# Kernel tuning notes

Measured on AMD Instinct MI355X. Metric: run time of the kernel, lower is better.

## Reference

```python
import jax, jax.numpy as jnp
import numpy as np

DIM = 1024
DEPTH = 4
HEADS = 16
MLP = 4096
B, N = 4, 1024
SCALE = DIM ** (-0.5)  # NOTE: module scales by dim^-0.5, not head_dim^-0.5
EPS = 1e-5


def setup_inputs() -> dict:
    key = jax.random.key(0)
    ks = jax.random.split(key, 13)
    s = 0.02
    return {
        "x": jax.random.normal(ks[0], (B, N, DIM), dtype=jnp.float32),
        "ln1_g": jnp.ones((DEPTH, DIM), jnp.float32),
        "ln1_b": jnp.zeros((DEPTH, DIM), jnp.float32),
        "w_qkv": jax.random.normal(ks[1], (DEPTH, DIM, 3 * DIM), jnp.float32) * s,
        "w_out": jax.random.normal(ks[2], (DEPTH, DIM, DIM), jnp.float32) * s,
        "b_out": jnp.zeros((DEPTH, DIM), jnp.float32),
        "ln2_g": jnp.ones((DEPTH, DIM), jnp.float32),
        "ln2_b": jnp.zeros((DEPTH, DIM), jnp.float32),
        "w1": jax.random.normal(ks[3], (DEPTH, DIM, MLP), jnp.float32) * s,
        "b1": jnp.zeros((DEPTH, MLP), jnp.float32),
        "w2": jax.random.normal(ks[4], (DEPTH, MLP, DIM), jnp.float32) * s,
        "b2": jnp.zeros((DEPTH, DIM), jnp.float32),
    }


def _layernorm(x, g, b):
    m = jnp.mean(x, axis=-1, keepdims=True)
    v = jnp.mean(jnp.square(x - m), axis=-1, keepdims=True)
    return (x - m) * jax.lax.rsqrt(v + EPS) * g + b


def _gelu(x):
    # x * 0.5 * (1 + erf(x / sqrt(2)))  (exact GeLu from the module)
    return x * 0.5 * (1.0 + jax.lax.erf(x / jnp.sqrt(2.0).astype(x.dtype)))


def _block(x, p):
    ln1_g, ln1_b, w_qkv, w_out, b_out, ln2_g, ln2_b, w1, b1, w2, b2 = p
    # --- attention (pre-norm, residual) ---
    h = _layernorm(x, ln1_g, ln1_b)
    qkv = h @ w_qkv  # [b, n, 3*dim]
    q, k, v = jnp.split(qkv, 3, axis=-1)
    def heads(t):  # [b, n, dim] -> [b, h, n, d]
        b_, n_, _ = t.shape
        return t.reshape(b_, n_, HEADS, DIM // HEADS).transpose(0, 2, 1, 3)
    q, k, v = heads(q), heads(k), heads(v)
    dots = jnp.einsum('bhid,bhjd->bhij', q, k) * SCALE
    attn = jax.nn.softmax(dots, axis=-1)
    o = jnp.einsum('bhij,bhjd->bhid', attn, v)
    o = o.transpose(0, 2, 1, 3).reshape(x.shape)  # [b, n, dim]
    x = x + (o @ w_out + b_out)
    # --- feed-forward (pre-norm, residual) ---
    h = _layernorm(x, ln2_g, ln2_b)
    x = x + (_gelu(h @ w1 + b1) @ w2 + b2)
    return x


def reference(x, ln1_g, ln1_b, w_qkv, w_out, b_out, ln2_g, ln2_b, w1, b1, w2, b2):
    for l in range(DEPTH):
        p = (ln1_g[l], ln1_b[l], w_qkv[l], w_out[l], b_out[l],
             ln2_g[l], ln2_b[l], w1[l], b1[l], w2[l], b2[l])
        x = _block(x, p)
    return x
```

## Files before the change

kernel.cpp:

```cpp
#include <hip/hip_runtime.h>

typedef __bf16 bf16;
typedef __bf16 bf16x4 __attribute__((ext_vector_type(4)));
typedef __bf16 bf16x8 __attribute__((ext_vector_type(8)));
typedef float  f32x4  __attribute__((ext_vector_type(4)));

#define DIMV   1024
#define MLPV   4096
#define MROWS  4096
#define NHEAD  16
#define SCALEV 0.03125f
#define QKV_LD 3072
#define MB (1024ull * 1024ull)

__device__ __forceinline__ void gload16(const bf16* g, bf16* l) {
    __builtin_amdgcn_global_load_lds((const __attribute__((address_space(1))) unsigned int*)g,
                                     (__attribute__((address_space(3))) unsigned int*)l,
                                     16, 0, 0);
}

__global__ __launch_bounds__(256) void k_ln(const float* __restrict__ x,
                                            const float* __restrict__ g,
                                            const float* __restrict__ b,
                                            bf16* __restrict__ h) {
    int row = blockIdx.x;
    int tid = threadIdx.x;
    const f32x4 v = ((const f32x4*)(x + (size_t)row * DIMV))[tid];
    float s  = v[0]+v[1]+v[2]+v[3];
    float sq = v[0]*v[0]+v[1]*v[1]+v[2]*v[2]+v[3]*v[3];
    for (int m = 1; m < 64; m <<= 1) { s += __shfl_xor(s, m, 64); sq += __shfl_xor(sq, m, 64); }
    __shared__ float ss[4], ssq[4];
    int w = tid >> 6, lane = tid & 63;
    if (lane == 0) { ss[w] = s; ssq[w] = sq; }
    __syncthreads();
    s  = ss[0]+ss[1]+ss[2]+ss[3];
    sq = ssq[0]+ssq[1]+ssq[2]+ssq[3];
    float mean = s * (1.f/DIMV);
    float var  = sq * (1.f/DIMV) - mean*mean;
    float rs   = rsqrtf(var + 1e-5f);
    int c0 = tid * 4;
    const f32x4 gv = ((const f32x4*)(g))[tid];
    const f32x4 bv = ((const f32x4*)(b))[tid];
    bf16x4 o;
    for (int i = 0; i < 4; i++)
        o[i] = (bf16)((v[i]-mean)*rs*gv[i] + bv[i]);
    *(bf16x4*)(h + (size_t)row * DIMV + c0) = o;
}

__global__ __launch_bounds__(256) void k_transpose_cvt(const float* __restrict__ in,
                                                       bf16* __restrict__ out, int R, int C) {
    __shared__ float tile[32][33];
    int tx = threadIdx.x & 31, ty = threadIdx.x >> 5;
    int r0 = blockIdx.y * 32, c0 = blockIdx.x * 32;
    for (int i = 0; i < 4; i++)
        tile[ty + 8*i][tx] = in[(size_t)(r0 + ty + 8*i) * C + c0 + tx];
    __syncthreads();
    for (int i = 0; i < 4; i++)
        out[(size_t)(c0 + ty + 8*i) * R + r0 + tx] = (bf16)tile[tx][ty + 8*i];
}

template<int EPI, int TN>
__global__ __launch_bounds__(256) void k_gemm(const bf16* __restrict__ A,
                                              const bf16* __restrict__ Bt,
                                              const float* __restrict__ bias,
                                              bf16* __restrict__ Cb,
                                              float* __restrict__ Cacc,
                                              int N, int K) {
    constexpr int NWN = TN / 64;
    constexpr int MT  = (TN == 128) ? 4 : 2;
    __shared__ alignas(16) bf16 As[2][128 * 64];
    __shared__ alignas(16) bf16 Bs[2][TN * 64];
    const int tid  = threadIdx.x;
    const int lane = tid & 63, w = tid >> 6;
    const int quad = lane >> 4, l16 = lane & 15;
    const int wm = w / NWN, wn = w % NWN;

    const int gx   = (int)gridDim.x;
    const int nwg  = gx * (int)gridDim.y;
    const int orig = (int)blockIdx.y * gx + (int)blockIdx.x;
    const int qq = nwg >> 3, rr = nwg & 7;
    const int xcd = orig & 7, loc = orig >> 3;
    const int wg  = (xcd < rr ? xcd * (qq + 1) : rr * (qq + 1) + (xcd - rr) * qq) + loc;
    const int bn = wg % gx, bm = wg / gx;

    const bf16* Ag = A  + (size_t)bm * 128 * K;
    const bf16* Bg = Bt + (size_t)bn * TN * K;

    const int srow = lane >> 3;
    const int scol = lane & 7;
    const int sswz = (scol ^ srow) << 3;

    f32x4 acc[MT][4];
    f32x4 zero = {0.f,0.f,0.f,0.f};
    for (int mt = 0; mt < MT; mt++) for (int nt = 0; nt < 4; nt++) acc[mt][nt] = zero;

    auto stage = [&](int p, int k0) {
        #pragma unroll
        for (int i = 0; i < 4; i++) {
            int row = w * 32 + i * 8;
            gload16(&Ag[(size_t)(row + srow) * K + k0 + sswz], &As[p][row * 64]);
        }
        #pragma unroll
        for (int i = 0; i < TN / 32; i++) {
            int row = w * (TN / 4) + i * 8;
            gload16(&Bg[(size_t)(row + srow) * K + k0 + sswz], &Bs[p][row * 64]);
        }
    };

    const int NT = K >> 6;
    stage(0, 0);
    __syncthreads();

    for (int t = 0; t < NT; t++) {
        const int p = t & 1;
        if (t + 1 < NT) stage(p ^ 1, (t + 1) << 6);

        bf16x8 af[MT][2], bfr[4][2];
        #pragma unroll
        for (int mt = 0; mt < MT; mt++)
            #pragma unroll
            for (int ks = 0; ks < 2; ks++) {
                int row = wm * (MT * 16) + mt * 16 + l16;
                int kb  = ks * 4 + quad;
                af[mt][ks] = *(const bf16x8*)&As[p][row * 64 + ((kb ^ (row & 7)) << 3)];
            }
        #pragma unroll
        for (int nt = 0; nt < 4; nt++)
            #pragma unroll
            for (int ks = 0; ks < 2; ks++) {
                int row = wn * 64 + nt * 16 + l16;
                int kb  = ks * 4 + quad;
                bfr[nt][ks] = *(const bf16x8*)&Bs[p][row * 64 + ((kb ^ (row & 7)) << 3)];
            }
        #pragma unroll
        for (int ks = 0; ks < 2; ks++)
            #pragma unroll
            for (int mt = 0; mt < MT; mt++)
                #pragma unroll
                for (int nt = 0; nt < 4; nt++)
                    acc[mt][nt] = __builtin_amdgcn_mfma_f32_16x16x32_bf16(af[mt][ks], bfr[nt][ks], acc[mt][nt], 0, 0, 0);

        __syncthreads();
    }

    for (int mt = 0; mt < MT; mt++) for (int nt = 0; nt < 4; nt++) {
        int col = bn * TN + wn * 64 + nt * 16 + l16;
        float bval = (EPI >= 1) ? bias[col] : 0.f;
        for (int r = 0; r < 4; r++) {
            int row = bm * 128 + wm * (MT * 16) + mt * 16 + quad * 4 + r;
            float v = acc[mt][nt][r];
            if (EPI == 0) {
                Cb[(size_t)row * N + col] = (bf16)v;
            } else if (EPI == 1) {
                float t = v + bval;
                float ge = 0.5f * t * (1.f + erff(t * 0.70710678118f));
                Cb[(size_t)row * N + col] = (bf16)ge;
            } else {
                Cacc[(size_t)row * N + col] += v + bval;
            }
        }
    }
}

__global__ __launch_bounds__(256) void k_attn(const bf16* __restrict__ qkv, bf16* __restrict__ o) {
    const int qt = blockIdx.x;
    const int h  = blockIdx.y;
    const int bb = blockIdx.z;
    const int tid  = threadIdx.x;
    const int lane = tid & 63, w = tid >> 6;
    const int quad = lane >> 4, l16 = lane & 15;

    __shared__ alignas(16) bf16 Qs[128 * 72];
    __shared__ alignas(16) bf16 Ks[64 * 72];
    __shared__ alignas(16) bf16 Vt[64 * 72];
    __shared__ alignas(16) bf16 Ps[128 * 72];

    const bf16* qbase = qkv + (size_t)(bb*1024 + qt*128) * QKV_LD + h*64;

    for (int c = tid; c < 1024; c += 256) {
        int r = c >> 3, cb = (c & 7) * 8;
        *(bf16x8*)&Qs[r * 72 + cb] = *(const bf16x8*)&qbase[(size_t)r * QKV_LD + cb];
    }

    f32x4 o_acc[2][4];
    f32x4 zero = {0.f,0.f,0.f,0.f};
    for (int mt = 0; mt < 2; mt++) for (int nt = 0; nt < 4; nt++) o_acc[mt][nt] = zero;
    float l_st[2][4];
    for (int mt = 0; mt < 2; mt++) for (int r = 0; r < 4; r++) l_st[mt][r] = 0.f;

    const int vj = tid >> 2;
    const int vd0 = (tid & 3) * 16;

    for (int kt = 0; kt < 16; kt++) {
        const bf16* kbase = qkv + (size_t)(bb*1024 + kt*64) * QKV_LD + 1024 + h*64;
        const bf16* vbase = qkv + (size_t)(bb*1024 + kt*64) * QKV_LD + 2048 + h*64;
        for (int c = tid; c < 512; c += 256) {
            int r = c >> 3, cb = (c & 7) * 8;
            *(bf16x8*)&Ks[r * 72 + cb] = *(const bf16x8*)&kbase[(size_t)r * QKV_LD + cb];
        }
        {
            bf16x8 v0 = *(const bf16x8*)&vbase[(size_t)vj * QKV_LD + vd0];
            bf16x8 v1 = *(const bf16x8*)&vbase[(size_t)vj * QKV_LD + vd0 + 8];
            #pragma unroll
            for (int i = 0; i < 8; i++) {
                Vt[(vd0 + i) * 72 + vj]     = v0[i];
                Vt[(vd0 + 8 + i) * 72 + vj] = v1[i];
            }
        }
        __syncthreads();

        f32x4 sv[2][4];
        for (int mt = 0; mt < 2; mt++) for (int nt = 0; nt < 4; nt++) {
            f32x4 a = zero;
            for (int ks = 0; ks < 2; ks++) {
                bf16x8 qf = *(const bf16x8*)&Qs[(w*32 + mt*16 + l16) * 72 + ks*32 + quad*8];
                bf16x8 kf = *(const bf16x8*)&Ks[(nt*16 + l16) * 72 + ks*32 + quad*8];
                a = __builtin_amdgcn_mfma_f32_16x16x32_bf16(qf, kf, a, 0, 0, 0);
            }
            for (int r = 0; r < 4; r++) sv[mt][nt][r] = a[r] * SCALEV;
        }

        for (int mt = 0; mt < 2; mt++) for (int r = 0; r < 4; r++) {
            float rs = 0.f;
            for (int nt = 0; nt < 4; nt++) {
                float p = __expf(sv[mt][nt][r]);
                sv[mt][nt][r] = p;
                rs += p;
            }
            for (int msk = 1; msk < 16; msk <<= 1) rs += __shfl_xor(rs, msk, 64);
            l_st[mt][r] += rs;
        }

        for (int mt = 0; mt < 2; mt++) for (int nt = 0; nt < 4; nt++)
            for (int r = 0; r < 4; r++)
                Ps[(w*32 + mt*16 + quad*4 + r) * 72 + nt*16 + l16] = (bf16)sv[mt][nt][r];
        __syncthreads();

        for (int mt = 0; mt < 2; mt++) for (int nt = 0; nt < 4; nt++) {
            f32x4 a = o_acc[mt][nt];
            for (int ks = 0; ks < 2; ks++) {
                bf16x8 pf = *(const bf16x8*)&Ps[(w*32 + mt*16 + l16) * 72 + ks*32 + quad*8];
                bf16x8 vf = *(const bf16x8*)&Vt[(nt*16 + l16) * 72 + ks*32 + quad*8];
                a = __builtin_amdgcn_mfma_f32_16x16x32_bf16(pf, vf, a, 0, 0, 0);
            }
            o_acc[mt][nt] = a;
        }
        __syncthreads();
    }

    for (int mt = 0; mt < 2; mt++) for (int nt = 0; nt < 4; nt++)
        for (int r = 0; r < 4; r++) {
            float val = o_acc[mt][nt][r] / l_st[mt][r];
            int row = qt*128 + w*32 + mt*16 + quad*4 + r;
            o[(size_t)(bb*1024 + row) * DIMV + h*64 + nt*16 + l16] = (bf16)val;
        }
}

extern "C" void kernel_launch(void* const* d_in, const int* in_sizes, int n_in,
                              void* d_out, int out_size, void* d_ws, size_t ws_size,
                              hipStream_t stream) {
    (void)in_sizes; (void)n_in; (void)out_size;
    const float* x_in  = (const float*)d_in[0];
    const float* ln1_g = (const float*)d_in[1];
    const float* ln1_b = (const float*)d_in[2];
    const float* w_qkv = (const float*)d_in[3];
    const float* w_out = (const float*)d_in[4];
    const float* b_out = (const float*)d_in[5];
    const float* ln2_g = (const float*)d_in[6];
    const float* ln2_b = (const float*)d_in[7];
    const float* w1    = (const float*)d_in[8];
    const float* b1    = (const float*)d_in[9];
    const float* w2    = (const float*)d_in[10];
    const float* b2    = (const float*)d_in[11];

    char* ws = (char*)d_ws;
    float* xf32    = (float*)ws;
    bf16*  h       = (bf16*)(ws + 16*MB);
    bf16*  wT1     = (bf16*)(ws + 24*MB);
    bf16*  wT2     = (bf16*)(ws + 32*MB);
    bf16*  attn_o  = (bf16*)(ws + 40*MB);
    bf16*  big     = (bf16*)(ws + 48*MB);
    size_t bigsz   = (ws_size > 48*MB) ? (ws_size - 48*MB) : 0;

    int G = 4;
    while (G > 1 && (size_t)G * 6*MB > bigsz) G >>= 1;
    int RC = 4096;
    while (RC > 128 && (size_t)RC * 8192ull > bigsz) RC >>= 1;

    hipMemcpyAsync(xf32, x_in, (size_t)MROWS * DIMV * sizeof(float),
                   hipMemcpyDeviceToDevice, stream);

    for (int l = 0; l < 4; l++) {
        k_ln<<<MROWS, 256, 0, stream>>>(xf32, ln1_g + (size_t)l*DIMV, ln1_b + (size_t)l*DIMV, h);
        k_transpose_cvt<<<dim3(3072/32, 1024/32), 256, 0, stream>>>(w_qkv + (size_t)l*DIMV*3072, wT1, 1024, 3072);
        for (int g = 0; g < 4; g += G) {
            k_gemm<0,128><<<dim3(3072/128, (G*1024)/128), 256, 0, stream>>>(
                h + (size_t)g*1024*DIMV, wT1, (const float*)nullptr, big, (float*)nullptr, 3072, 1024);
            k_attn<<<dim3(8, NHEAD, G), 256, 0, stream>>>(big, attn_o + (size_t)g*1024*DIMV);
        }
        k_transpose_cvt<<<dim3(1024/32, 1024/32), 256, 0, stream>>>(w_out + (size_t)l*DIMV*DIMV, wT1, 1024, 1024);
        k_gemm<2,64><<<dim3(1024/64, 4096/128), 256, 0, stream>>>(
            attn_o, wT1, b_out + (size_t)l*DIMV, (bf16*)nullptr, xf32, 1024, 1024);

        k_ln<<<MROWS, 256, 0, stream>>>(xf32, ln2_g + (size_t)l*DIMV, ln2_b + (size_t)l*DIMV, h);
        k_transpose_cvt<<<dim3(4096/32, 1024/32), 256, 0, stream>>>(w1 + (size_t)l*DIMV*MLPV, wT1, 1024, 4096);
        k_transpose_cvt<<<dim3(1024/32, 4096/32), 256, 0, stream>>>(w2 + (size_t)l*MLPV*DIMV, wT2, 4096, 1024);
        for (int r0 = 0; r0 < 4096; r0 += RC) {
            k_gemm<1,128><<<dim3(4096/128, RC/128), 256, 0, stream>>>(
                h + (size_t)r0*DIMV, wT1, b1 + (size_t)l*MLPV, big, (float*)nullptr, 4096, 1024);
            k_gemm<2,64><<<dim3(1024/64, RC/128), 256, 0, stream>>>(
                big, wT2, b2 + (size_t)l*DIMV, (bf16*)nullptr, xf32 + (size_t)r0*DIMV, 1024, 4096);
        }
    }

    hipMemcpyAsync(d_out, xf32, (size_t)MROWS * DIMV * sizeof(float),
                   hipMemcpyDeviceToDevice, stream);
}
```

Before: 1.265 ms.

## Pre-transpose V and double-buffer K/V with async LDS loads in attention

Adds a separate kernel that transposes V into a head-major buffer so the attention kernel no longer does a scalar scatter transpose into shared memory. The attention kernel now stages Q, K and V through direct global-to-LDS loads into XOR-swizzled tiles and double-buffers K/V so the next tile's loads overlap the current tile's MFMA work. It also drops one barrier and raises wave priority around the MFMA sections. In exchange it costs an extra kernel launch and a round trip of V through global memory, needs more workspace, and the barrier removal depends on the lgkmcnt wait alone ordering the Ps writes before they are read.

```diff
diff --git a/kernel.cpp b/kernel.cpp
--- a/kernel.cpp
+++ b/kernel.cpp
@@ -57,6 +57,19 @@
     __syncthreads();
     for (int i = 0; i < 4; i++)
         out[(size_t)(c0 + ty + 8*i) * R + r0 + tx] = (bf16)tile[tx][ty + 8*i];
+}
+
+__global__ __launch_bounds__(256) void k_vt(const bf16* __restrict__ big, bf16* __restrict__ vT) {
+    __shared__ bf16 tile[32][33];
+    int tx = threadIdx.x & 31, ty = threadIdx.x >> 5;
+    int hd0 = blockIdx.x * 32, s0 = blockIdx.y * 32, bb = blockIdx.z;
+    const bf16* src = big + (size_t)bb * 1024 * QKV_LD + 2048;
+    for (int i = 0; i < 4; i++)
+        tile[ty + 8*i][tx] = src[(size_t)(s0 + ty + 8*i) * QKV_LD + hd0 + tx];
+    __syncthreads();
+    bf16* dst = vT + (size_t)bb * 1024 * 1024;
+    for (int i = 0; i < 4; i++)
+        dst[(size_t)(hd0 + ty + 8*i) * 1024 + s0 + tx] = tile[tx][ty + 8*i];
 }
 
 template<int EPI, int TN>
@@ -162,25 +175,40 @@
     }
 }
 
-__global__ __launch_bounds__(256) void k_attn(const bf16* __restrict__ qkv, bf16* __restrict__ o) {
+__global__ __launch_bounds__(256) void k_attn(const bf16* __restrict__ qkv,
+                                              const bf16* __restrict__ vT,
+                                              bf16* __restrict__ o) {
     const int qt = blockIdx.x;
     const int h  = blockIdx.y;
     const int bb = blockIdx.z;
     const int tid  = threadIdx.x;
     const int lane = tid & 63, w = tid >> 6;
     const int quad = lane >> 4, l16 = lane & 15;
-
-    __shared__ alignas(16) bf16 Qs[128 * 72];
-    __shared__ alignas(16) bf16 Ks[64 * 72];
-    __shared__ alignas(16) bf16 Vt[64 * 72];
+    const int srow = lane >> 3, scol = lane & 7;
+    const int sswz = (scol ^ srow) << 3;
+
+    __shared__ alignas(16) bf16 Qs[128 * 64];
+    __shared__ alignas(16) bf16 Ks[2][64 * 64];
+    __shared__ alignas(16) bf16 Vs[2][64 * 64];
     __shared__ alignas(16) bf16 Ps[128 * 72];
 
-    const bf16* qbase = qkv + (size_t)(bb*1024 + qt*128) * QKV_LD + h*64;
-
-    for (int c = tid; c < 1024; c += 256) {
-        int r = c >> 3, cb = (c & 7) * 8;
-        *(bf16x8*)&Qs[r * 72 + cb] = *(const bf16x8*)&qbase[(size_t)r * QKV_LD + cb];
-    }
+    const bf16* qbase  = qkv + (size_t)(bb*1024 + qt*128) * QKV_LD + h*64;
+    const bf16* kbase0 = qkv + (size_t)(bb*1024) * QKV_LD + 1024 + h*64;
+    const bf16* vbase0 = vT  + ((size_t)bb*1024 + h*64) * 1024;
+
+    #pragma unroll
+    for (int i = 0; i < 4; i++) {
+        int row = w * 32 + i * 8;
+        gload16(&qbase[(size_t)(row + srow) * QKV_LD + sswz], &Qs[row * 64]);
+    }
+    auto stageKV = [&](int p, int kt) {
+        #pragma unroll
+        for (int i = 0; i < 2; i++) {
+            int row = w * 16 + i * 8;
+            gload16(&kbase0[(size_t)(kt*64 + row + srow) * QKV_LD + sswz], &Ks[p][row * 64]);
+            gload16(&vbase0[(size_t)(row + srow) * 1024 + kt*64 + sswz],   &Vs[p][row * 64]);
+        }
+    };
 
     f32x4 o_acc[2][4];
     f32x4 zero = {0.f,0.f,0.f,0.f};
@@ -188,44 +216,34 @@
     float l_st[2][4];
     for (int mt = 0; mt < 2; mt++) for (int r = 0; r < 4; r++) l_st[mt][r] = 0.f;
 
-    const int vj = tid >> 2;
-    const int vd0 = (tid & 3) * 16;
+    stageKV(0, 0);
+    __syncthreads();
 
     for (int kt = 0; kt < 16; kt++) {
-        const bf16* kbase = qkv + (size_t)(bb*1024 + kt*64) * QKV_LD + 1024 + h*64;
-        const bf16* vbase = qkv + (size_t)(bb*1024 + kt*64) * QKV_LD + 2048 + h*64;
-        for (int c = tid; c < 512; c += 256) {
-            int r = c >> 3, cb = (c & 7) * 8;
-            *(bf16x8*)&Ks[r * 72 + cb] = *(const bf16x8*)&kbase[(size_t)r * QKV_LD + cb];
-        }
-        {
-            bf16x8 v0 = *(const bf16x8*)&vbase[(size_t)vj * QKV_LD + vd0];
-            bf16x8 v1 = *(const bf16x8*)&vbase[(size_t)vj * QKV_LD + vd0 + 8];
-            #pragma unroll
-            for (int i = 0; i < 8; i++) {
-                Vt[(vd0 + i) * 72 + vj]     = v0[i];
-                Vt[(vd0 + 8 + i) * 72 + vj] = v1[i];
-            }
-        }
-        __syncthreads();
+        const int p = kt & 1;
+        if (kt < 15) stageKV(p ^ 1, kt + 1);
 
         f32x4 sv[2][4];
+        __builtin_amdgcn_s_setprio(1);
         for (int mt = 0; mt < 2; mt++) for (int nt = 0; nt < 4; nt++) {
             f32x4 a = zero;
+            #pragma unroll
             for (int ks = 0; ks < 2; ks++) {
-                bf16x8 qf = *(const bf16x8*)&Qs[(w*32 + mt*16 + l16) * 72 + ks*32 + quad*8];
-                bf16x8 kf = *(const bf16x8*)&Ks[(nt*16 + l16) * 72 + ks*32 + quad*8];
+                int kb = ks * 4 + quad;
+                bf16x8 qf = *(const bf16x8*)&Qs[(w*32 + mt*16 + l16) * 64 + ((kb ^ (l16 & 7)) << 3)];
+                bf16x8 kf = *(const bf16x8*)&Ks[p][(nt*16 + l16) * 64 + ((kb ^ (l16 & 7)) << 3)];
                 a = __builtin_amdgcn_mfma_f32_16x16x32_bf16(qf, kf, a, 0, 0, 0);
             }
-            for (int r = 0; r < 4; r++) sv[mt][nt][r] = a[r] * SCALEV;
-        }
+            sv[mt][nt] = a;
+        }
+        __builtin_amdgcn_s_setprio(0);
 
         for (int mt = 0; mt < 2; mt++) for (int r = 0; r < 4; r++) {
             float rs = 0.f;
             for (int nt = 0; nt < 4; nt++) {
-                float p = __expf(sv[mt][nt][r]);
-                sv[mt][nt][r] = p;
-                rs += p;
+                float pe = __expf(sv[mt][nt][r] * SCALEV);
+                sv[mt][nt][r] = pe;
+                rs += pe;
             }
             for (int msk = 1; msk < 16; msk <<= 1) rs += __shfl_xor(rs, msk, 64);
             l_st[mt][r] += rs;
@@ -234,17 +252,23 @@
         for (int mt = 0; mt < 2; mt++) for (int nt = 0; nt < 4; nt++)
             for (int r = 0; r < 4; r++)
                 Ps[(w*32 + mt*16 + quad*4 + r) * 72 + nt*16 + l16] = (bf16)sv[mt][nt][r];
-        __syncthreads();
-
+        asm volatile("s_waitcnt lgkmcnt(0)" ::: "memory");
+        __builtin_amdgcn_sched_barrier(0);
+
+        __builtin_amdgcn_s_setprio(1);
         for (int mt = 0; mt < 2; mt++) for (int nt = 0; nt < 4; nt++) {
             f32x4 a = o_acc[mt][nt];
+            #pragma unroll
             for (int ks = 0; ks < 2; ks++) {
+                int kb = ks * 4 + quad;
                 bf16x8 pf = *(const bf16x8*)&Ps[(w*32 + mt*16 + l16) * 72 + ks*32 + quad*8];
-                bf16x8 vf = *(const bf16x8*)&Vt[(nt*16 + l16) * 72 + ks*32 + quad*8];
+                bf16x8 vf = *(const bf16x8*)&Vs[p][(nt*16 + l16) * 64 + ((kb ^ (l16 & 7)) << 3)];
                 a = __builtin_amdgcn_mfma_f32_16x16x32_bf16(pf, vf, a, 0, 0, 0);
             }
             o_acc[mt][nt] = a;
         }
+        __builtin_amdgcn_s_setprio(0);
+
         __syncthreads();
     }
 
@@ -283,9 +307,11 @@
     size_t bigsz   = (ws_size > 48*MB) ? (ws_size - 48*MB) : 0;
 
     int G = 4;
-    while (G > 1 && (size_t)G * 6*MB > bigsz) G >>= 1;
+    while (G > 1 && (size_t)G * 8*MB > bigsz) G >>= 1;
     int RC = 4096;
     while (RC > 128 && (size_t)RC * 8192ull > bigsz) RC >>= 1;
+
+    bf16* vT = big + (size_t)G * 1024 * QKV_LD;
 
     hipMemcpyAsync(xf32, x_in, (size_t)MROWS * DIMV * sizeof(float),
                    hipMemcpyDeviceToDevice, stream);
@@ -296,7 +322,8 @@
         for (int g = 0; g < 4; g += G) {
             k_gemm<0,128><<<dim3(3072/128, (G*1024)/128), 256, 0, stream>>>(
                 h + (size_t)g*1024*DIMV, wT1, (const float*)nullptr, big, (float*)nullptr, 3072, 1024);
-            k_attn<<<dim3(8, NHEAD, G), 256, 0, stream>>>(big, attn_o + (size_t)g*1024*DIMV);
+            k_vt<<<dim3(32, 32, G), 256, 0, stream>>>(big, vT);
+            k_attn<<<dim3(8, NHEAD, G), 256, 0, stream>>>(big, vT, attn_o + (size_t)g*1024*DIMV);
         }
         k_transpose_cvt<<<dim3(1024/32, 1024/32), 256, 0, stream>>>(w_out + (size_t)l*DIMV*DIMV, wT1, 1024, 1024);
         k_gemm<2,64><<<dim3(1024/64, 4096/128), 256, 0, stream>>>(
```

Result: faster. 1.233 ms (-2.5%).
